# Kernel tuning notes

Hardware: AMD Instinct MI355X
Metric: run time of the kernel (lower is better)

## Reference

```python
import jax, jax.numpy as jnp
import numpy as np

D_MSA = 256
D_PAIR = 128
N_HEADS = 8
HEAD_DIM = D_MSA // N_HEADS
EPS = 1e-5


def setup_inputs() -> dict:
    key = jax.random.key(0)
    ks = jax.random.split(key, 14)
    s = 0.02
    return {
        "msa": jax.random.normal(ks[0], (1, 64, 256, D_MSA), dtype=jnp.float32),
        "pair": jax.random.normal(ks[1], (1, 256, 256, D_PAIR), dtype=jnp.float32),
        "Wq": jax.random.normal(ks[2], (D_MSA, D_MSA), dtype=jnp.float32) * s,
        "bq": jnp.zeros((D_MSA,), jnp.float32),
        "Wk": jax.random.normal(ks[3], (D_MSA, D_MSA), dtype=jnp.float32) * s,
        "bk": jnp.zeros((D_MSA,), jnp.float32),
        "Wv": jax.random.normal(ks[4], (D_MSA, D_MSA), dtype=jnp.float32) * s,
        "bv": jnp.zeros((D_MSA,), jnp.float32),
        "Wpb": jax.random.normal(ks[5], (D_PAIR, N_HEADS), dtype=jnp.float32) * s,
        "bpb": jnp.zeros((N_HEADS,), jnp.float32),
        "Wo": jax.random.normal(ks[6], (D_MSA, D_MSA), dtype=jnp.float32) * s,
        "bo": jnp.zeros((D_MSA,), jnp.float32),
        "gamma": jnp.ones((D_MSA,), jnp.float32),
        "beta": jnp.zeros((D_MSA,), jnp.float32),
    }


def reference(msa, pair, Wq, bq, Wk, bk, Wv, bv, Wpb, bpb, Wo, bo, gamma, beta):
    B, N, L, D = msa.shape
    H, Hd = N_HEADS, HEAD_DIM
    # projections -> (B, N, L, H, Hd)
    q = (msa @ Wq + bq).reshape(B, N, L, H, Hd)
    k = (msa @ Wk + bk).reshape(B, N, L, H, Hd)
    v = (msa @ Wv + bv).reshape(B, N, L, H, Hd)
    # scores: (B, N, H, L, L)
    scores = jnp.einsum('bnihd,bnjhd->bnhij', q, k) / jnp.sqrt(jnp.float32(Hd))
    # pair bias: (B, L, L, H) -> (B, H, L, L), broadcast over N
    pb = jnp.transpose(pair @ Wpb + bpb, (0, 3, 1, 2))
    scores = scores + pb[:, None]
    attn = jax.nn.softmax(scores, axis=-1)
    attn_out = jnp.einsum('bnhij,bnjhd->bnihd', attn, v).reshape(B, N, L, D)
    attn_out = attn_out @ Wo + bo
    # residual + LayerNorm
    x = msa + attn_out
    mu = jnp.mean(x, axis=-1, keepdims=True)
    var = jnp.var(x, axis=-1, keepdims=True)
    return (x - mu) * jax.lax.rsqrt(var + EPS) * gamma + beta
```

## Files before the change

### kernel.cpp

```cpp
#include <hip/hip_runtime.h>

#define NSEQ 64
#define LL   256
#define DD   256
#define HH   8
#define HDIM 32

typedef short short8  __attribute__((ext_vector_type(8)));
typedef short short4v __attribute__((ext_vector_type(4)));
typedef float float4v __attribute__((ext_vector_type(4)));

#define MFMA16(a,b,c) __builtin_amdgcn_mfma_f32_16x16x32_bf16((a),(b),(c),0,0,0)

__device__ __forceinline__ float4v zero4() {
  float4v z;
  z[0] = 0.f; z[1] = 0.f; z[2] = 0.f; z[3] = 0.f;
  return z;
}

__device__ __forceinline__ short f2b(float f) {
  unsigned u = __float_as_uint(f);
  u = (u + 0x7fffu + ((u >> 16) & 1u)) >> 16;
  return (short)u;
}

__device__ __forceinline__ float b2f(short s) {
  return __uint_as_float(((unsigned)(unsigned short)s) << 16);
}

__device__ __forceinline__ void ld_lds16(const void* g, void* l) {
  __builtin_amdgcn_global_load_lds(
      (const __attribute__((address_space(1))) unsigned int*)g,
      (__attribute__((address_space(3))) unsigned int*)l, 16, 0, 0);
}
#define WAIT_VM0() __builtin_amdgcn_s_waitcnt(0x0F70)

#define WT_OFF    0
#define PB_OFF    (4*65536*2)
#define PBF_OFF   (PB_OFF + 8*65536*2)
#define Q_OFF     (PB_OFF + 8*65536*4)
#define K_OFF     (Q_OFF  + 16384*256*2)
#define VT_OFF    (K_OFF  + 16384*256*2)
#define MSA16_OFF (VT_OFF + 16384*256*2)
#define O_OFF     MSA16_OFF

__global__ __launch_bounds__(256) void k1_prep(
    const float* __restrict__ msa,  const float* __restrict__ pair,
    const float* __restrict__ Wq,   const float* __restrict__ Wk,
    const float* __restrict__ Wv,   const float* __restrict__ Wpb,
    const float* __restrict__ bpb,  const float* __restrict__ Wo,
    char* __restrict__ ws)
{
  __shared__ __align__(16) short shm[4 * 64 * 128];
  __shared__ short ldsWt[16 * 136];
  int bx = blockIdx.x, tid = threadIdx.x;
  if (bx < 256) {
    short* pb16 = (short*)(ws + PB_OFF);
    for (int i = tid; i < 16 * 136; i += 256) ldsWt[i] = 0;
    __syncthreads();
    {
      float4 wv4 = *(const float4*)&Wpb[tid * 4];
      int kk = (tid * 4) >> 3, n0 = (tid * 4) & 7;
      ldsWt[(n0 + 0) * 136 + kk] = f2b(wv4.x);
      ldsWt[(n0 + 1) * 136 + kk] = f2b(wv4.y);
      ldsWt[(n0 + 2) * 136 + kk] = f2b(wv4.z);
      ldsWt[(n0 + 3) * 136 + kk] = f2b(wv4.w);
    }
    __syncthreads();
    int w = tid >> 6, l = tid & 63, q = l >> 4, c = l & 15;
    int base = bx * 256 + w * 64;
    short* lsWw = shm + w * 8192;
#pragma unroll
    for (int it = 0; it < 16; it++) {
      int jl = it * 4 + (l >> 4);
      int kc = l & 15;
      const float* src = &pair[(base + jl) * 128 + kc * 8];
      float4 a = *(const float4*)src;
      float4 b = *(const float4*)(src + 4);
      short8 v8;
      v8[0] = f2b(a.x); v8[1] = f2b(a.y); v8[2] = f2b(a.z); v8[3] = f2b(a.w);
      v8[4] = f2b(b.x); v8[5] = f2b(b.y); v8[6] = f2b(b.z); v8[7] = f2b(b.w);
      *(short8*)&lsWw[jl * 128 + ((kc ^ (jl & 7)) * 8)] = v8;
    }
    float bias = bpb[c & 7];
    short8 bf[4];
#pragma unroll
    for (int ks = 0; ks < 4; ks++)
      bf[ks] = *(const short8*)&ldsWt[c * 136 + ks * 32 + q * 8];
    float4v acc[4];
#pragma unroll
    for (int mt = 0; mt < 4; mt++) acc[mt] = zero4();
#pragma unroll
    for (int ks = 0; ks < 4; ks++) {
#pragma unroll
      for (int mt = 0; mt < 4; mt++) {
        int row = mt * 16 + c;
        short8 af = *(const short8*)&lsWw[row * 128 + (((ks * 4 + q) ^ (c & 7)) * 8)];
        acc[mt] = MFMA16(af, bf[ks], acc[mt]);
      }
    }
    if (c < 8) {
#pragma unroll
      for (int mt = 0; mt < 4; mt++) {
        short4v o;
#pragma unroll
        for (int r = 0; r < 4; r++) o[r] = f2b(acc[mt][r] + bias);
        *(short4v*)&pb16[c * 65536 + base + mt * 16 + q * 4] = o;
      }
    }
  } else if (bx < 320) {
    int b2 = bx - 256;
    int mat = b2 >> 4, sub = b2 & 15;
    int k0 = (sub >> 2) * 64, n0 = (sub & 3) * 64;
    const float* W = (mat == 0) ? Wq : (mat == 1) ? Wk : (mat == 2) ? Wv : Wo;
    short* wt = (short*)(ws + WT_OFF) + mat * 65536;
    short* ldsT = shm;
#pragma unroll
    for (int p = 0; p < 4; p++) {
      int kl = p * 16 + (tid >> 4);
      int nl = (tid & 15) * 4;
      float4 v = *(const float4*)&W[(k0 + kl) * 256 + n0 + nl];
      ldsT[(nl + 0) * 72 + kl] = f2b(v.x);
      ldsT[(nl + 1) * 72 + kl] = f2b(v.y);
      ldsT[(nl + 2) * 72 + kl] = f2b(v.z);
      ldsT[(nl + 3) * 72 + kl] = f2b(v.w);
    }
    __syncthreads();
#pragma unroll
    for (int p = 0; p < 2; p++) {
      int id = p * 256 + tid;
      int nl = id >> 3, c8 = id & 7;
      *(short8*)&wt[(n0 + nl) * 256 + k0 + c8 * 8] =
          *(const short8*)&ldsT[nl * 72 + c8 * 8];
    }
  } else {
    int b3 = bx - 320;
    const float* src = msa + b3 * 8192;
    short* dst = (short*)(ws + MSA16_OFF) + b3 * 8192;
#pragma unroll
    for (int i = 0; i < 8; i++) {
      int idx = i * 1024 + tid * 4;
      float4 v = *(const float4*)&src[idx];
      short4v s;
      s[0] = f2b(v.x); s[1] = f2b(v.y); s[2] = f2b(v.z); s[3] = f2b(v.w);
      *(short4v*)&dst[idx] = s;
    }
  }
}

__global__ __launch_bounds__(256) void k2_qkv(
    const float* __restrict__ bq, const float* __restrict__ bk,
    const float* __restrict__ bv, char* __restrict__ ws)
{
  __shared__ __align__(16) short ls[2 * 128 * 128];
  short* lsA = ls;
  short* lsB = ls + 16384;
  int bx = blockIdx.x, tid = threadIdx.x;
  if (bx >= 768) {
    int b = bx - 768;
    int it16 = b & 15;
    const short* src = (const short*)(ws + PB_OFF) + (b >> 4) * 65536 + it16 * 4096;
    short* pbf = (short*)(ws + PBF_OFF);
    short* lt = lsA;
#pragma unroll
    for (int i2 = 0; i2 < 2; i2++) {
      int idx = i2 * 2048 + tid * 8;
      *(short8*)&lt[(idx >> 8) * 264 + (idx & 255)] = *(const short8*)&src[idx];
    }
    __syncthreads();
#pragma unroll
    for (int i2 = 0; i2 < 4; i2++) {
      int fid = i2 * 256 + tid;
      int jt = fid >> 6, lane = fid & 63;
      int qp = lane >> 4, cp = lane & 15;
      short4v v;
#pragma unroll
      for (int r = 0; r < 4; r++)
        v[r] = lt[(qp * 4 + r) * 264 + jt * 16 + cp];
      *(short4v*)&pbf[((b * 16 + jt) * 64 + lane) * 4] = v;
    }
    return;
  }
  int rt = bx & 127, ct = bx >> 7;
  int m = ct >> 1, cb = (ct & 1) * 128;
  int R0 = rt * 128;
  const short* msa16 = (const short*)(ws + MSA16_OFF);
  const short* wt = (const short*)(ws + WT_OFF) + m * 65536;
  int w = tid >> 6, l = tid & 63, q = l >> 4, c = l & 15;
  int WR = (w & 1) * 64, WC = (w >> 1) * 64;
  float4v acc[4][4];
#pragma unroll
  for (int mt = 0; mt < 4; mt++)
#pragma unroll
    for (int nt = 0; nt < 4; nt++) acc[mt][nt] = zero4();

#pragma unroll 1
  for (int kk = 0; kk < 2; kk++) {
    if (kk) __syncthreads();
#pragma unroll
    for (int i = 0; i < 8; i++) {
      int ci = i * 256 + tid;
      int r = ci >> 4, pos = ci & 15;
      int kc = pos ^ (r & 7);
      ld_lds16(&msa16[(R0 + r) * 256 + kk * 128 + kc * 8], &lsA[ci * 8]);
    }
#pragma unroll
    for (int i = 0; i < 8; i++) {
      int ci = i * 256 + tid;
      int r = ci >> 4, pos = ci & 15;
      int kc = pos ^ (r & 7);
      ld_lds16(&wt[(cb + r) * 256 + kk * 128 + kc * 8], &lsB[ci * 8]);
    }
    WAIT_VM0();
    __syncthreads();
#pragma unroll
    for (int ks = 0; ks < 4; ks++) {
      short8 af[4], bf[4];
#pragma unroll
      for (int mt = 0; mt < 4; mt++) {
        int r = WR + mt * 16 + c;
        int phys = (ks * 4 + q) ^ (r & 7);
        af[mt] = *(const short8*)&lsA[r * 128 + phys * 8];
      }
#pragma unroll
      for (int nt = 0; nt < 4; nt++) {
        int r = WC + nt * 16 + c;
        int phys = (ks * 4 + q) ^ (r & 7);
        bf[nt] = *(const short8*)&lsB[r * 128 + phys * 8];
      }
#pragma unroll
      for (int mt = 0; mt < 4; mt++)
#pragma unroll
        for (int nt = 0; nt < 4; nt++)
          acc[mt][nt] = MFMA16(af[mt], bf[nt], acc[mt][nt]);
    }
  }

  const float* bp = (m == 0) ? bq : (m == 1) ? bk : bv;
  int n = R0 >> 8;
  __syncthreads();
  short* lsC = ls;
  if (m < 2) {
#pragma unroll
    for (int nt = 0; nt < 4; nt++) {
      float bb = bp[cb + WC + nt * 16 + c];
#pragma unroll
      for (int mt = 0; mt < 4; mt++)
#pragma unroll
        for (int r = 0; r < 4; r++)
          lsC[(WR + mt * 16 + q * 4 + r) * 136 + WC + nt * 16 + c] =
              f2b(acc[mt][nt][r] + bb);
    }
    __syncthreads();
    short* dst = (short*)(ws + (m == 0 ? Q_OFF : K_OFF)) + n * 65536;
    int ibase = R0 & 255;
#pragma unroll
    for (int p = 0; p < 8; p++) {
      int id = p * 256 + tid;
      int il = id >> 4, ch8 = id & 15;
      int chg = cb + ch8 * 8;
      int hh = chg >> 5, hd0 = chg & 31;
      *(short8*)&dst[(hh * 256 + ibase + il) * 32 + hd0] =
          *(const short8*)&lsC[il * 136 + ch8 * 8];
    }
  } else {
#pragma unroll
    for (int nt = 0; nt < 4; nt++) {
      float bb = bp[cb + WC + nt * 16 + c];
#pragma unroll
      for (int mt = 0; mt < 4; mt++)
#pragma unroll
        for (int r = 0; r < 4; r++)
          lsC[(WC + nt * 16 + c) * 136 + WR + mt * 16 + q * 4 + r] =
              f2b(acc[mt][nt][r] + bb);
    }
    __syncthreads();
    short* vt = (short*)(ws + VT_OFF) + n * 65536;
    int jbase = R0 & 255;
#pragma unroll
    for (int p = 0; p < 8; p++) {
      int id = p * 256 + tid;
      int chl = id >> 4, j8 = id & 15;
      int chg = cb + chl;
      *(short8*)&vt[chg * 256 + jbase + j8 * 8] =
          *(const short8*)&lsC[chl * 136 + j8 * 8];
    }
  }
}

__global__ __launch_bounds__(256) void k3_attn(char* __restrict__ ws)
{
  __shared__ __align__(16) short lds[25088];
  short* lsK = lds;
  short* lsP = lds;
  short* lsV = lds + 16896;
  int bx = blockIdx.x, tid = threadIdx.x;
  int qq = bx >> 9, grp = bx & 511;
  int n = grp >> 3, h = grp & 7;
  int w = tid >> 6, l = tid & 63, q = l >> 4, c = l & 15;
  const short* qh = (const short*)(ws + Q_OFF) + (n * HH + h) * 256 * HDIM;
  const short* kh = (const short*)(ws + K_OFF) + (n * HH + h) * 256 * HDIM;
  const short* vt = (const short*)(ws + VT_OFF) + (n * HH + h) * HDIM * 256;
  const short* pbf = (const short*)(ws + PBF_OFF) + (h * 16 + qq * 4 + w) * 16 * 256;
  short* os = (short*)(ws + O_OFF);
  const float scale = 0.17677669529663687f;
  int i0 = qq * 64 + w * 16;

  short8 aq = *(const short8*)&qh[(i0 + c) * HDIM + q * 8];

#pragma unroll
  for (int i = 0; i < 4; i++) {
    int ci = i * 256 + tid;
    ld_lds16(&kh[ci * 8], &lsK[ci * 8]);
  }
#pragma unroll
  for (int i = 0; i < 4; i++) {
    int ci = i * 256 + tid;
    int row = ci >> 5, j = ci & 31;
    int sj = j ^ (row & 7);
    ld_lds16(&vt[row * 256 + sj * 8], &lsV[ci * 8]);
  }
  WAIT_VM0();
  __syncthreads();

  float4v s[16];
#pragma unroll
  for (int jt = 0; jt < 16; jt++) {
    short8 bk8 = *(const short8*)&lsK[(jt * 16 + c) * 32 + q * 8];
    s[jt] = MFMA16(aq, bk8, zero4());
  }
#pragma unroll
  for (int jt = 0; jt < 16; jt++) {
    short4v pv = *(const short4v*)&pbf[(jt * 64 + l) * 4];
#pragma unroll
    for (int r = 0; r < 4; r++)
      s[jt][r] = __builtin_fmaf(s[jt][r], scale, b2f(pv[r]));
  }
  float inv[4];
#pragma unroll
  for (int r = 0; r < 4; r++) {
    float m = s[0][r];
#pragma unroll
    for (int jt = 1; jt < 16; jt++) m = fmaxf(m, s[jt][r]);
    m = fmaxf(m, __shfl_xor(m, 1, 64));
    m = fmaxf(m, __shfl_xor(m, 2, 64));
    m = fmaxf(m, __shfl_xor(m, 4, 64));
    m = fmaxf(m, __shfl_xor(m, 8, 64));
    float rs = 0.f;
#pragma unroll
    for (int jt = 0; jt < 16; jt++) {
      float p = __expf(s[jt][r] - m);
      s[jt][r] = p;
      rs += p;
    }
    rs += __shfl_xor(rs, 1, 64);
    rs += __shfl_xor(rs, 2, 64);
    rs += __shfl_xor(rs, 4, 64);
    rs += __shfl_xor(rs, 8, 64);
    inv[r] = 1.f / rs;
  }
  __syncthreads();
#pragma unroll
  for (int jt = 0; jt < 16; jt++)
#pragma unroll
    for (int r = 0; r < 4; r++)
      lsP[(w * 16 + q * 4 + r) * 264 + jt * 16 + c] = f2b(s[jt][r]);
  float4v o0 = zero4(), o1 = zero4();
#pragma unroll
  for (int kk = 0; kk < 8; kk++) {
    short8 ap = *(const short8*)&lsP[(w * 16 + c) * 264 + kk * 32 + q * 8];
    int sl0 = ((kk * 4 + q) ^ (c & 7)) * 8;
    short8 b0 = *(const short8*)&lsV[c * 256 + sl0];
    short8 b1 = *(const short8*)&lsV[(16 + c) * 256 + sl0];
    o0 = MFMA16(ap, b0, o0);
    o1 = MFMA16(ap, b1, o1);
  }
#pragma unroll
  for (int r = 0; r < 4; r++) {
    os[(n * 256 + i0 + q * 4 + r) * 256 + h * 32 + c]      = f2b(o0[r] * inv[r]);
    os[(n * 256 + i0 + q * 4 + r) * 256 + h * 32 + 16 + c] = f2b(o1[r] * inv[r]);
  }
}

__global__ __launch_bounds__(256) void k4_out(
    const float* __restrict__ msa, const float* __restrict__ bo,
    const float* __restrict__ gamma, const float* __restrict__ beta,
    const char* __restrict__ ws, float* __restrict__ out)
{
  __shared__ __align__(16) short lsA[32 * 128];
  __shared__ __align__(16) short lsB[256 * 128];
  __shared__ float sred[2][32][2];
  int bx = blockIdx.x, tid = threadIdx.x;
  int w = tid >> 6, l = tid & 63, q = l >> 4, c = l & 15;
  int rg = w >> 1, ch2 = w & 1;
  int R0 = bx * 32;
  int Rw = R0 + rg * 16;
  int C0 = ch2 * 128;
  const short* osrc = (const short*)(ws + O_OFF);
  const short* wto  = (const short*)(ws + WT_OFF) + 3 * 65536;

  float4v acc[8];
#pragma unroll
  for (int nt = 0; nt < 8; nt++) acc[nt] = zero4();

#pragma unroll 1
  for (int kk = 0; kk < 2; kk++) {
    if (kk) __syncthreads();
#pragma unroll
    for (int i = 0; i < 2; i++) {
      int ci = i * 256 + tid;
      int r = ci >> 4, pos = ci & 15;
      int kc = pos ^ (r & 7);
      ld_lds16(&osrc[(R0 + r) * 256 + kk * 128 + kc * 8], &lsA[ci * 8]);
    }
#pragma unroll
    for (int i = 0; i < 16; i++) {
      int ci = i * 256 + tid;
      int r = ci >> 4, pos = ci & 15;
      int kc = pos ^ (r & 7);
      ld_lds16(&wto[r * 256 + kk * 128 + kc * 8], &lsB[ci * 8]);
    }
    WAIT_VM0();
    __syncthreads();
#pragma unroll
    for (int ks = 0; ks < 4; ks++) {
      int rA = rg * 16 + c;
      int physA = (ks * 4 + q) ^ (rA & 7);
      short8 af = *(const short8*)&lsA[rA * 128 + physA * 8];
#pragma unroll
      for (int nt = 0; nt < 8; nt++) {
        int rB = C0 + nt * 16 + c;
        int phys = (ks * 4 + q) ^ (rB & 7);
        short8 bf = *(const short8*)&lsB[rB * 128 + phys * 8];
        acc[nt] = MFMA16(af, bf, acc[nt]);
      }
    }
  }

  float s1[4] = {0, 0, 0, 0}, s2[4] = {0, 0, 0, 0};
#pragma unroll
  for (int nt = 0; nt < 8; nt++) {
    float bb = bo[C0 + nt * 16 + c];
#pragma unroll
    for (int r = 0; r < 4; r++) {
      float x = acc[nt][r] + bb + msa[(Rw + q * 4 + r) * 256 + C0 + nt * 16 + c];
      acc[nt][r] = x;
      s1[r] += x;
      s2[r] = __builtin_fmaf(x, x, s2[r]);
    }
  }
#pragma unroll
  for (int r = 0; r < 4; r++) {
    s1[r] += __shfl_xor(s1[r], 1, 64); s2[r] += __shfl_xor(s2[r], 1, 64);
    s1[r] += __shfl_xor(s1[r], 2, 64); s2[r] += __shfl_xor(s2[r], 2, 64);
    s1[r] += __shfl_xor(s1[r], 4, 64); s2[r] += __shfl_xor(s2[r], 4, 64);
    s1[r] += __shfl_xor(s1[r], 8, 64); s2[r] += __shfl_xor(s2[r], 8, 64);
  }
  if (c == 0) {
#pragma unroll
    for (int r = 0; r < 4; r++) {
      sred[0][rg * 16 + q * 4 + r][ch2] = s1[r];
      sred[1][rg * 16 + q * 4 + r][ch2] = s2[r];
    }
  }
  __syncthreads();
  float mu[4], rsd[4];
#pragma unroll
  for (int r = 0; r < 4; r++) {
    int row = rg * 16 + q * 4 + r;
    float a = sred[0][row][0] + sred[0][row][1];
    float b = sred[1][row][0] + sred[1][row][1];
    float m = a * (1.f / 256.f);
    float v = __builtin_fmaf(-m, m, b * (1.f / 256.f));
    mu[r] = m;
    rsd[r] = rsqrtf(v + 1e-5f);
  }
#pragma unroll
  for (int nt = 0; nt < 8; nt++) {
    float g = gamma[C0 + nt * 16 + c], bt = beta[C0 + nt * 16 + c];
#pragma unroll
    for (int r = 0; r < 4; r++)
      out[(Rw + q * 4 + r) * 256 + C0 + nt * 16 + c] =
          (acc[nt][r] - mu[r]) * rsd[r] * g + bt;
  }
}

extern "C" void kernel_launch(void* const* d_in, const int* in_sizes, int n_in,
                              void* d_out, int out_size, void* d_ws, size_t ws_size,
                              hipStream_t stream)
{
  const float* msa   = (const float*)d_in[0];
  const float* pair  = (const float*)d_in[1];
  const float* Wq    = (const float*)d_in[2];
  const float* bq    = (const float*)d_in[3];
  const float* Wk    = (const float*)d_in[4];
  const float* bk    = (const float*)d_in[5];
  const float* Wv    = (const float*)d_in[6];
  const float* bv    = (const float*)d_in[7];
  const float* Wpb   = (const float*)d_in[8];
  const float* bpb   = (const float*)d_in[9];
  const float* Wo    = (const float*)d_in[10];
  const float* bo    = (const float*)d_in[11];
  const float* gamma = (const float*)d_in[12];
  const float* beta  = (const float*)d_in[13];
  char* ws = (char*)d_ws;
  float* out = (float*)d_out;

  hipLaunchKernelGGL(k1_prep, dim3(832), dim3(256), 0, stream,
                     msa, pair, Wq, Wk, Wv, Wpb, bpb, Wo, ws);
  hipLaunchKernelGGL(k2_qkv, dim3(896), dim3(256), 0, stream,
                     bq, bk, bv, ws);
  hipLaunchKernelGGL(k3_attn, dim3(2048), dim3(256), 0, stream, ws);
  hipLaunchKernelGGL(k4_out, dim3(512), dim3(256), 0, stream,
                     msa, bo, gamma, beta, ws, out);
}
```

Measured before the change: 158.0 us.

## Transpose attention MFMA operands so softmax rows live per lane, use exp2

Swaps the A/B operands of the QK^T and PV MFMAs so each lane holds a query row's scores across registers. The softmax max and sum can then mostly reduce in registers with only two cross-lane shuffles. The pair-bias layout is transposed to match, and log2(e) is folded into the bias and scale so exp2 can replace exp. P is packed with v_cvt_pk_bf16 into vector LDS stores, and outputs are written as short4 vectors instead of scalar stores.

```diff
diff --git a/kernel.cpp b/kernel.cpp
--- a/kernel.cpp
+++ b/kernel.cpp
@@ -26,6 +26,12 @@
 
 __device__ __forceinline__ float b2f(short s) {
   return __uint_as_float(((unsigned)(unsigned short)s) << 16);
+}
+
+__device__ __forceinline__ unsigned pkbf(float a, float b) {
+  unsigned r;
+  asm volatile("v_cvt_pk_bf16_f32 %0, %1, %2" : "=v"(r) : "v"(a), "v"(b));
+  return r;
 }
 
 __device__ __forceinline__ void ld_lds16(const void* g, void* l) {
@@ -104,7 +110,8 @@
       for (int mt = 0; mt < 4; mt++) {
         short4v o;
 #pragma unroll
-        for (int r = 0; r < 4; r++) o[r] = f2b(acc[mt][r] + bias);
+        for (int r = 0; r < 4; r++)
+          o[r] = f2b((acc[mt][r] + bias) * 1.44269504088896f);
         *(short4v*)&pb16[c * 65536 + base + mt * 16 + q * 4] = o;
       }
     }
@@ -173,10 +180,7 @@
       int fid = i2 * 256 + tid;
       int jt = fid >> 6, lane = fid & 63;
       int qp = lane >> 4, cp = lane & 15;
-      short4v v;
-#pragma unroll
-      for (int r = 0; r < 4; r++)
-        v[r] = lt[(qp * 4 + r) * 264 + jt * 16 + cp];
+      short4v v = *(const short4v*)&lt[cp * 264 + jt * 16 + qp * 4];
       *(short4v*)&pbf[((b * 16 + jt) * 64 + lane) * 4] = v;
     }
     return;
@@ -303,7 +307,7 @@
   const short* vt = (const short*)(ws + VT_OFF) + (n * HH + h) * HDIM * 256;
   const short* pbf = (const short*)(ws + PBF_OFF) + (h * 16 + qq * 4 + w) * 16 * 256;
   short* os = (short*)(ws + O_OFF);
-  const float scale = 0.17677669529663687f;
+  const float scl2 = 0.17677669529663687f * 1.44269504088896f;
   int i0 = qq * 64 + w * 16;
 
   short8 aq = *(const short8*)&qh[(i0 + c) * HDIM + q * 8];
@@ -326,60 +330,69 @@
   float4v s[16];
 #pragma unroll
   for (int jt = 0; jt < 16; jt++) {
-    short8 bk8 = *(const short8*)&lsK[(jt * 16 + c) * 32 + q * 8];
-    s[jt] = MFMA16(aq, bk8, zero4());
+    short8 kf = *(const short8*)&lsK[(jt * 16 + c) * 32 + q * 8];
+    s[jt] = MFMA16(kf, aq, zero4());
   }
 #pragma unroll
   for (int jt = 0; jt < 16; jt++) {
     short4v pv = *(const short4v*)&pbf[(jt * 64 + l) * 4];
 #pragma unroll
     for (int r = 0; r < 4; r++)
-      s[jt][r] = __builtin_fmaf(s[jt][r], scale, b2f(pv[r]));
-  }
-  float inv[4];
-#pragma unroll
-  for (int r = 0; r < 4; r++) {
-    float m = s[0][r];
-#pragma unroll
-    for (int jt = 1; jt < 16; jt++) m = fmaxf(m, s[jt][r]);
-    m = fmaxf(m, __shfl_xor(m, 1, 64));
-    m = fmaxf(m, __shfl_xor(m, 2, 64));
-    m = fmaxf(m, __shfl_xor(m, 4, 64));
-    m = fmaxf(m, __shfl_xor(m, 8, 64));
-    float rs = 0.f;
-#pragma unroll
-    for (int jt = 0; jt < 16; jt++) {
-      float p = __expf(s[jt][r] - m);
-      s[jt][r] = p;
-      rs += p;
-    }
-    rs += __shfl_xor(rs, 1, 64);
-    rs += __shfl_xor(rs, 2, 64);
-    rs += __shfl_xor(rs, 4, 64);
-    rs += __shfl_xor(rs, 8, 64);
-    inv[r] = 1.f / rs;
-  }
+      s[jt][r] = __builtin_fmaf(s[jt][r], scl2, b2f(pv[r]));
+  }
+  float t[16];
+#pragma unroll
+  for (int jt = 0; jt < 16; jt++)
+    t[jt] = fmaxf(fmaxf(s[jt][0], s[jt][1]), fmaxf(s[jt][2], s[jt][3]));
+#pragma unroll
+  for (int st = 8; st >= 1; st >>= 1)
+#pragma unroll
+    for (int i = 0; i < st; i++) t[i] = fmaxf(t[i], t[i + st]);
+  float m = fmaxf(t[0], __shfl_xor(t[0], 16, 64));
+  m = fmaxf(m, __shfl_xor(m, 32, 64));
+#pragma unroll
+  for (int jt = 0; jt < 16; jt++) {
+#pragma unroll
+    for (int r = 0; r < 4; r++) s[jt][r] = exp2f(s[jt][r] - m);
+    t[jt] = (s[jt][0] + s[jt][1]) + (s[jt][2] + s[jt][3]);
+  }
+#pragma unroll
+  for (int st = 8; st >= 1; st >>= 1)
+#pragma unroll
+    for (int i = 0; i < st; i++) t[i] += t[i + st];
+  float rs = t[0];
+  rs += __shfl_xor(rs, 16, 64);
+  rs += __shfl_xor(rs, 32, 64);
+  float inv = 1.f / rs;
+
   __syncthreads();
-#pragma unroll
-  for (int jt = 0; jt < 16; jt++)
-#pragma unroll
-    for (int r = 0; r < 4; r++)
-      lsP[(w * 16 + q * 4 + r) * 264 + jt * 16 + c] = f2b(s[jt][r]);
+  int prow = (w * 16 + c) * 264;
+#pragma unroll
+  for (int jt = 0; jt < 16; jt++) {
+    uint2 u;
+    u.x = pkbf(s[jt][0], s[jt][1]);
+    u.y = pkbf(s[jt][2], s[jt][3]);
+    *(uint2*)&lsP[prow + jt * 16 + q * 4] = u;
+  }
   float4v o0 = zero4(), o1 = zero4();
 #pragma unroll
   for (int kk = 0; kk < 8; kk++) {
-    short8 ap = *(const short8*)&lsP[(w * 16 + c) * 264 + kk * 32 + q * 8];
+    short8 pf = *(const short8*)&lsP[prow + kk * 32 + q * 8];
     int sl0 = ((kk * 4 + q) ^ (c & 7)) * 8;
     short8 b0 = *(const short8*)&lsV[c * 256 + sl0];
     short8 b1 = *(const short8*)&lsV[(16 + c) * 256 + sl0];
-    o0 = MFMA16(ap, b0, o0);
-    o1 = MFMA16(ap, b1, o1);
-  }
+    o0 = MFMA16(b0, pf, o0);
+    o1 = MFMA16(b1, pf, o1);
+  }
+  short* orow = &os[(n * 256 + i0 + c) * 256 + h * 32];
+  short4v t0, t1;
 #pragma unroll
   for (int r = 0; r < 4; r++) {
-    os[(n * 256 + i0 + q * 4 + r) * 256 + h * 32 + c]      = f2b(o0[r] * inv[r]);
-    os[(n * 256 + i0 + q * 4 + r) * 256 + h * 32 + 16 + c] = f2b(o1[r] * inv[r]);
-  }
+    t0[r] = f2b(o0[r] * inv);
+    t1[r] = f2b(o1[r] * inv);
+  }
+  *(short4v*)&orow[q * 4] = t0;
+  *(short4v*)&orow[16 + q * 4] = t1;
 }
 
 __global__ __launch_bounds__(256) void k4_out(
```

New measurement: 158.0 us. No clear change (-0.0%).
